# Performance work log

Measured on AMD Instinct MI355X. Metric: run time of the kernel, lower is better.

The kernel has to match this reference:

```python
import jax, jax.numpy as jnp
import numpy as np

B, N, D_IN, D_OUT, H, W = 2, 2048, 1024, 1024, 16, 64
DH = D_OUT // H


def setup_inputs() -> dict:
    key = jax.random.key(0)
    ks = jax.random.split(key, 6)
    x = jax.random.normal(ks[0], (B, N, D_IN), dtype=jnp.float32)
    s_in = 1.0 / np.sqrt(D_IN)
    s_out = 1.0 / np.sqrt(D_OUT)
    wq = jax.random.normal(ks[1], (D_IN, D_OUT), dtype=jnp.float32) * s_in
    wk = jax.random.normal(ks[2], (D_IN, D_OUT), dtype=jnp.float32) * s_in
    wv = jax.random.normal(ks[3], (D_IN, D_OUT), dtype=jnp.float32) * s_in
    wo = jax.random.normal(ks[4], (D_OUT, D_OUT), dtype=jnp.float32) * s_out
    # sparse global tokens: every 256th token is global
    global_attention = (jnp.arange(N)[None, :] % 256 == 0) & jnp.ones((B, 1), bool)
    return {"x": x, "wq": wq, "wk": wk, "wv": wv, "wo": wo,
            "global_attention": global_attention}


def _mask(global_attention):
    # True = masked out. Causal local window + global rows/cols unmasked.
    i = jnp.arange(N)[:, None]
    j = jnp.arange(N)[None, :]
    allowed = (i - j < W) & (i >= j)          # causal sliding window
    local_mask = ~allowed                      # [N, N], True = masked
    g = global_attention                       # [B, N] bool
    # global token j clears row j and column j of the mask
    global_clear = g[:, :, None] | g[:, None, :]   # [B, N, N]
    return local_mask[None, :, :] & ~global_clear  # [B, N, N]


def reference(x, wq, wk, wv, wo, global_attention):
    b, n, _ = x.shape
    q = (x @ wq).reshape(b, n, H, DH).transpose(0, 2, 1, 3)  # [b,h,n,dh]
    k = (x @ wk).reshape(b, n, H, DH).transpose(0, 2, 1, 3)
    v = (x @ wv).reshape(b, n, H, DH).transpose(0, 2, 1, 3)
    scores = jnp.einsum('bhqd,bhkd->bhqk', q, k) / jnp.sqrt(jnp.float32(DH))
    mask = _mask(global_attention)[:, None, :, :]            # [b,1,n,n]
    scores = jnp.where(mask, -jnp.inf, scores)
    attn = jax.nn.softmax(scores, axis=-1)
    ctx = jnp.einsum('bhqk,bhkd->bqhd', attn, v).reshape(b, n, D_OUT)
    return ctx @ wo
```

## Files before the change

kernel.cpp:

```cpp
#include <hip/hip_runtime.h>


using u16 = unsigned short;
using u32 = unsigned int;

typedef __attribute__((ext_vector_type(8))) short bf16x8;
typedef __attribute__((ext_vector_type(4))) float f32x4;

__device__ __forceinline__ float b2f(u16 s) {
  union { u32 u; float f; } x; x.u = ((u32)s) << 16; return x.f;
}
__device__ __forceinline__ u16 f2b(float f) {
  union { float f; u32 u; } x; x.f = f;
  u32 r = (x.u + 0x7fffu + ((x.u >> 16) & 1u)) >> 16;
  return (u16)r;
}

__global__ __launch_bounds__(256) void k_pre(const float* __restrict__ x,
                                             u16* __restrict__ xb,
                                             const float* __restrict__ wq,
                                             const float* __restrict__ wk,
                                             const float* __restrict__ wv,
                                             const float* __restrict__ wo,
                                             u16* __restrict__ wqkvT,
                                             u16* __restrict__ woT) {
  __shared__ float tile[64][65];
  const int bid = blockIdx.x;
  if (bid < 2048) {
    int idx = (bid * 256 + threadIdx.x) * 8;
    float4 a = *(const float4*)(x + idx);
    float4 b = *(const float4*)(x + idx + 4);
    uint4 o;
    o.x = (u32)f2b(a.x) | ((u32)f2b(a.y) << 16);
    o.y = (u32)f2b(a.z) | ((u32)f2b(a.w) << 16);
    o.z = (u32)f2b(b.x) | ((u32)f2b(b.y) << 16);
    o.w = (u32)f2b(b.z) | ((u32)f2b(b.w) << 16);
    *(uint4*)(xb + idx) = o;
  } else {
    const int id = bid - 2048;
    const int z = id >> 8, xy = id & 255;
    const float* src = (z == 0) ? wq : (z == 1) ? wk : (z == 2) ? wv : wo;
    u16* dst = (z < 3) ? (wqkvT + ((size_t)z << 20)) : woT;
    const int n0 = (xy & 15) * 64, k0 = (xy >> 4) * 64;
    const int tx = threadIdx.x & 63, ty = threadIdx.x >> 6;
    #pragma unroll
    for (int r = 0; r < 64; r += 4)
      tile[r + ty][tx] = src[(size_t)(k0 + r + ty) * 1024 + n0 + tx];
    __syncthreads();
    #pragma unroll
    for (int r = 0; r < 64; r += 4)
      dst[(size_t)(n0 + r + ty) * 1024 + k0 + tx] = f2b(tile[tx][r + ty]);
  }
}

__device__ __forceinline__ void gload16(const u16* g, u16* l) {
  __builtin_amdgcn_global_load_lds((const __attribute__((address_space(1))) void*)g,
                                   (__attribute__((address_space(3))) void*)l, 16, 0, 0);
}

__global__ __launch_bounds__(512, 2) void k_qkv256(const u16* __restrict__ A,
                                                   const u16* __restrict__ Bt,
                                                   u16* __restrict__ C) {
  __shared__ __attribute__((aligned(16))) u16 lds[57344];
  const int K = 1024, N = 3072, NT = 16;
  const int t = threadIdx.x;
  const int wid = t >> 6, lane = t & 63;
  const int l4 = lane >> 4, l16 = lane & 15;
  const int qr = wid >> 1, qc = wid & 1;
  const int d = blockIdx.y * gridDim.x + blockIdx.x;
  const int qq = (gridDim.x * gridDim.y) >> 3;
  const int tau = (d & 7) * qq + (d >> 3);
  const int bn = tau % gridDim.x, bm = tau / gridDim.x;
  const u16* Ab = A + (size_t)bm * 256 * K;
  const u16* Bb = Bt + (size_t)bn * 192 * K;
  const int rowbase = wid * 8 + (lane >> 3);
  const int qcg = rowbase >> 5, rrb = rowbase & 31;
  const int scc = ((lane & 7) ^ ((lane >> 3) & 7)) << 3;
  const int rsw = (l16 & 7);
  f32x4 acc[3][4][2] = {};
  bf16x8 af[4][2], bf[2][2];

  #define STG_A(BUF, KT, H)                                                        \
    { u16* lb = lds + (BUF) * 16384 + (H) * 8192 + (wid << 9);                     \
      _Pragma("unroll")                                                            \
      for (int i = 0; i < 2; ++i)                                                  \
        gload16(Ab + (size_t)((H) * 128 + i * 64 + rowbase) * K + (KT) * 64 + scc, \
                lb + i * 4096); }

  #define STG_B1(BUF, KT, I)                                                       \
    { u16* lb = lds + 32768 + (BUF) * 12288 + (I) * 4096 + (wid << 9);             \
      gload16(Bb + (size_t)(qcg * 96 + (I) * 32 + rrb) * K + (KT) * 64 + scc, lb); }

  #define LOAD_A(AS)                                                               \
    { _Pragma("unroll")                                                            \
      for (int m = 0; m < 4; ++m) {                                                \
        const int ro = qr * 64 + m * 16 + l16;                                     \
        _Pragma("unroll")                                                          \
        for (int ks = 0; ks < 2; ++ks)                                             \
          af[m][ks] = *(const bf16x8*)&(AS)[ro * 64 + (((ks * 4 + l4) ^ rsw) << 3)]; \
      } }

  #define LOAD_B(BS, NH)                                                           \
    { _Pragma("unroll")                                                            \
      for (int n = 0; n < 2; ++n) {                                                \
        const int po = (NH) * 64 + qc * 32 + n * 16 + l16;                         \
        _Pragma("unroll")                                                          \
        for (int ks = 0; ks < 2; ++ks)                                             \
          bf[n][ks] = *(const bf16x8*)&(BS)[po * 64 + (((ks * 4 + l4) ^ rsw) << 3)]; \
      } }

  #define QUAD(NH)                                                                 \
    { __builtin_amdgcn_s_setprio(1);                                               \
      _Pragma("unroll")                                                            \
      for (int m = 0; m < 4; ++m)                                                  \
        _Pragma("unroll")                                                          \
        for (int n = 0; n < 2; ++n) {                                              \
          f32x4 c = acc[NH][m][n];                                                 \
          c = __builtin_amdgcn_mfma_f32_16x16x32_bf16(af[m][0], bf[n][0], c, 0, 0, 0); \
          c = __builtin_amdgcn_mfma_f32_16x16x32_bf16(af[m][1], bf[n][1], c, 0, 0, 0); \
          acc[NH][m][n] = c;                                                       \
        }                                                                          \
      __builtin_amdgcn_s_setprio(0); }

  STG_A(0, 0, 0); STG_A(0, 0, 1);
  STG_B1(0, 0, 0); STG_B1(0, 0, 1); STG_B1(0, 0, 2);
  STG_A(1, 1, 0); STG_A(1, 1, 1);
  STG_B1(1, 1, 0);
  asm volatile("s_waitcnt vmcnt(5)" ::: "memory");
  __builtin_amdgcn_s_barrier();

  for (int tt = 0; tt < NT; ++tt) {
    const int beta = tt & 1;
    const u16* As = lds + beta * 16384;
    const u16* Bs = lds + 32768 + beta * 12288;
    LOAD_A(As);
    LOAD_B(Bs, 0);
    if (tt + 1 < NT) STG_B1(beta ^ 1, tt + 1, 1);
    __builtin_amdgcn_s_barrier();
    QUAD(0);
    __builtin_amdgcn_s_barrier();
    LOAD_B(Bs, 1);
    if (tt + 1 < NT) STG_B1(beta ^ 1, tt + 1, 2);
    __builtin_amdgcn_s_barrier();
    QUAD(1);
    __builtin_amdgcn_s_barrier();
    LOAD_B(Bs, 2);
    if (tt + 2 < NT) {
      STG_A(beta, tt + 2, 0);
      STG_A(beta, tt + 2, 1);
      STG_B1(beta, tt + 2, 0);
    }
    __builtin_amdgcn_s_barrier();
    QUAD(2);
    if (tt + 2 < NT)      asm volatile("s_waitcnt vmcnt(5)" ::: "memory");
    else if (tt + 1 < NT) asm volatile("s_waitcnt vmcnt(0)" ::: "memory");
    __builtin_amdgcn_s_barrier();
  }
  #undef STG_A
  #undef STG_B1
  #undef LOAD_A
  #undef LOAD_B
  #undef QUAD

  #pragma unroll
  for (int nh = 0; nh < 3; ++nh)
    #pragma unroll
    for (int m = 0; m < 4; ++m) {
      const int row0 = bm * 256 + qr * 64 + m * 16 + l4 * 4;
      #pragma unroll
      for (int n = 0; n < 2; ++n) {
        const int col = bn * 192 + qc * 96 + nh * 32 + n * 16 + l16;
        #pragma unroll
        for (int r = 0; r < 4; ++r)
          C[(size_t)(row0 + r) * N + col] = f2b(acc[nh][m][n][r]);
      }
    }
}

__global__ __launch_bounds__(512, 2) void k_out(const u16* __restrict__ A,
                                                const u16* __restrict__ Bt,
                                                float* __restrict__ C,
                                                const float* __restrict__ gpart,
                                                u16* __restrict__ ctxw) {
  __shared__ __attribute__((aligned(16))) u16 lds[32768];
  const int K = 1024, N = 1024, NT = 16;
  const int t = threadIdx.x;
  const int wid = t >> 6, lane = t & 63;
  const int l4 = lane >> 4, l16 = lane & 15;
  const int qr = wid >> 2, qc = wid & 3;
  const int d = blockIdx.y * gridDim.x + blockIdx.x;
  const int qq = (gridDim.x * gridDim.y) >> 3;
  const int tau = (d & 7) * qq + (d >> 3);
  const int bn = tau % gridDim.x, bm = tau / gridDim.x;
  const u16* Ab = A + (size_t)bm * 128 * K;
  const u16* Bb = Bt + (size_t)bn * 128 * K;
  const int rowbase = wid * 8 + (lane >> 3);
  const int qcg = rowbase >> 4, rrb = rowbase & 15;
  const int scc = ((lane & 7) ^ ((lane >> 3) & 7)) << 3;
  const int rsw = (l16 & 7);
  f32x4 acc[2][4] = {};
  bf16x8 af[4][2], bf[2][2];

  if ((bm & 1) == 0) {
    if (t < 256) {
      const int bb = bm >> 4;
      const int irow = (bm & 15) * 128;
      const int row8 = (bm & 15) >> 1;
      const int h = t >> 4;
      const int d0 = (t & 15) * 4;
      const float* g0 = gpart + ((size_t)(bb * 16 + h) * 32) * 520;
      float o0 = 0.f, o1 = 0.f, o2 = 0.f, o3 = 0.f, ls = 0.f;
      for (int q = 0; q < 32; ++q) {
        const float4 v = *(const float4*)(g0 + q * 520 + row8 * 64 + d0);
        o0 += v.x; o1 += v.y; o2 += v.z; o3 += v.w;
        ls += g0[q * 520 + 512 + row8];
      }
      const float inv = 1.f / ls;
      u16* cw = ctxw + ((size_t)(bb * 2048 + irow)) * 1024 + h * 64 + d0;
      cw[0] = f2b(o0 * inv); cw[1] = f2b(o1 * inv);
      cw[2] = f2b(o2 * inv); cw[3] = f2b(o3 * inv);
    }
    __syncthreads();
  }

  #define OSTG_A(BUF, KT)                                                          \
    { u16* lb = lds + (BUF) * 8192 + (wid << 9);                                   \
      _Pragma("unroll")                                                            \
      for (int i = 0; i < 2; ++i)                                                  \
        gload16(Ab + (size_t)(i * 64 + rowbase) * K + (KT) * 64 + scc,             \
                lb + i * 4096); }

  #define OSTG_B(BUF, KT)                                                          \
    { u16* lb = lds + 16384 + (BUF) * 8192 + (wid << 9);                           \
      _Pragma("unroll")                                                            \
      for (int nf = 0; nf < 2; ++nf)                                               \
        gload16(Bb + (size_t)(qcg * 32 + nf * 16 + rrb) * K + (KT) * 64 + scc,     \
                lb + nf * 4096); }

  #define OLOAD()                                                                  \
    { _Pragma("unroll")                                                            \
      for (int m = 0; m < 4; ++m) {                                                \
        const int ro = qr * 64 + m * 16 + l16;                                     \
        _Pragma("unroll")                                                          \
        for (int ks = 0; ks < 2; ++ks)                                             \
          af[m][ks] = *(const bf16x8*)&As[ro * 64 + (((ks * 4 + l4) ^ rsw) << 3)]; \
      }                                                                            \
      _Pragma("unroll")                                                            \
      for (int nf = 0; nf < 2; ++nf) {                                             \
        const int po = nf * 64 + qc * 16 + l16;                                    \
        _Pragma("unroll")                                                          \
        for (int ks = 0; ks < 2; ++ks)                                             \
          bf[nf][ks] = *(const bf16x8*)&Bs[po * 64 + (((ks * 4 + l4) ^ rsw) << 3)]; \
      } }

  OSTG_A(0, 0); OSTG_B(0, 0);
  OSTG_A(1, 1); OSTG_B(1, 1);
  asm volatile("s_waitcnt vmcnt(4)" ::: "memory");
  __builtin_amdgcn_s_barrier();

  for (int tt = 0; tt < NT; ++tt) {
    const int beta = tt & 1;
    const u16* As = lds + beta * 8192;
    const u16* Bs = lds + 16384 + beta * 8192;
    OLOAD();
    asm volatile("s_waitcnt lgkmcnt(0)" ::: "memory");
    __builtin_amdgcn_s_barrier();
    if (tt + 2 < NT) { OSTG_A(beta, tt + 2); OSTG_B(beta, tt + 2); }
    __builtin_amdgcn_s_setprio(1);
    #pragma unroll
    for (int nf = 0; nf < 2; ++nf)
      #pragma unroll
      for (int m = 0; m < 4; ++m) {
        f32x4 c = acc[nf][m];
        c = __builtin_amdgcn_mfma_f32_16x16x32_bf16(af[m][0], bf[nf][0], c, 0, 0, 0);
        c = __builtin_amdgcn_mfma_f32_16x16x32_bf16(af[m][1], bf[nf][1], c, 0, 0, 0);
        acc[nf][m] = c;
      }
    __builtin_amdgcn_s_setprio(0);
    if (tt + 2 < NT)      asm volatile("s_waitcnt vmcnt(4)" ::: "memory");
    else if (tt + 1 < NT) asm volatile("s_waitcnt vmcnt(0)" ::: "memory");
    __builtin_amdgcn_s_barrier();
  }
  #undef OSTG_A
  #undef OSTG_B
  #undef OLOAD

  #pragma unroll
  for (int nf = 0; nf < 2; ++nf)
    #pragma unroll
    for (int m = 0; m < 4; ++m) {
      const int row0 = bm * 128 + qr * 64 + m * 16 + l4 * 4;
      const int col = bn * 128 + qc * 32 + nf * 16 + l16;
      #pragma unroll
      for (int r = 0; r < 4; ++r)
        C[(size_t)(row0 + r) * N + col] = acc[nf][m][r];
    }
}

__global__ __launch_bounds__(256) void k_attn_tile(const u16* __restrict__ qkv,
                                                   u16* __restrict__ ctx,
                                                   float* __restrict__ gpart) {
  __shared__ u16 buf[26880];
  __shared__ u16 Qgs[16 * 72];
  __shared__ u16 Pgs[16 * 72];
  __shared__ float lred[4][16];
  u16* Qs = buf;
  u16* Ks = buf + 4608;
  u16* Vt = buf + 16128;
  u16* Ps = buf;

  const int t = threadIdx.x, wid = t >> 6, lane = t & 63;
  const int l4 = lane >> 4, l16 = lane & 15;
  const int qt = blockIdx.x, h = blockIdx.y, b = blockIdx.z;
  const int q0 = qt * 64;
  const int kbase = q0 - 64;
  const size_t base = (size_t)b * 2048 * 3072;
  const u16* Qg = qkv + base + h * 64;
  const u16* Kg = qkv + base + 1024 + h * 64;
  const u16* Vg = qkv + base + 2048 + h * 64;

  for (int s = t; s < 512; s += 256) {
    int r = s >> 3, c = (s & 7) * 8;
    *(uint4*)&Qs[r * 72 + c] = *(const uint4*)&Qg[(size_t)(q0 + r) * 3072 + c];
  }
  if (t < 128) {
    int r = t >> 3, c = (t & 7) * 8;
    if (r < 8) {
      *(uint4*)&Qgs[r * 72 + c] = *(const uint4*)&Qg[(size_t)(r * 256) * 3072 + c];
    } else {
      uint4 z = {0, 0, 0, 0};
      *(uint4*)&Qgs[r * 72 + c] = z;
    }
  }
  for (int s = t; s < 1088; s += 256) {
    int r = s >> 3, c = (s & 7) * 8;
    int j = (r < 128) ? max(kbase + r, 0) : (r - 128) * 256;
    *(uint4*)&Ks[r * 72 + c] = *(const uint4*)&Kg[(size_t)j * 3072 + c];
  }
  for (int s = t; s < 1088; s += 256) {
    int r = s >> 3, c = (s & 7) * 8;
    int j = (r < 128) ? max(kbase + r, 0) : (r - 128) * 256;
    uint4 v = *(const uint4*)&Vg[(size_t)j * 3072 + c];
    const u16* pv = (const u16*)&v;
    const int ch = r >> 3;
    #pragma unroll
    for (int e8 = 0; e8 < 8; ++e8) {
      const int d = c + e8;
      const int kd = ((d >> 3) ^ d) & 7;
      const int chs = (ch < 16) ? (ch ^ kd) : ch;
      Vt[d * 168 + chs * 8 + (r & 7)] = pv[e8];
    }
  }
  for (int z = t; z < 64 * 24; z += 256) {
    int d = z / 24, j = 136 + z % 24;
    Vt[d * 168 + j] = 0;
  }
  __syncthreads();

  f32x4 sa[10] = {};
  #pragma unroll
  for (int ks = 0; ks < 2; ++ks) {
    bf16x8 qa = *(const bf16x8*)&Qs[(wid * 16 + l16) * 72 + ks * 32 + l4 * 8];
    #pragma unroll
    for (int n = 0; n < 10; ++n) {
      bf16x8 kb = *(const bf16x8*)&Ks[(n * 16 + l16) * 72 + ks * 32 + l4 * 8];
      sa[n] = __builtin_amdgcn_mfma_f32_16x16x32_bf16(qa, kb, sa[n], 0, 0, 0);
    }
  }

  f32x4 sg = {};
  #pragma unroll
  for (int ks = 0; ks < 2; ++ks) {
    bf16x8 qa = *(const bf16x8*)&Qgs[l16 * 72 + ks * 32 + l4 * 8];
    bf16x8 kb = *(const bf16x8*)&Ks[(64 + wid * 16 + l16) * 72 + ks * 32 + l4 * 8];
    sg = __builtin_amdgcn_mfma_f32_16x16x32_bf16(qa, kb, sg, 0, 0, 0);
  }
  #pragma unroll
  for (int r = 0; r < 4; ++r) {
    float p = __expf(sg[r] * 0.125f);
    sg[r] = p;
    #pragma unroll
    for (int o = 1; o < 16; o <<= 1) p += __shfl_xor(p, o);
    if (l16 == 0) lred[wid][l4 * 4 + r] = p;
  }
  #pragma unroll
  for (int r = 0; r < 4; ++r)
    Pgs[(l4 * 4 + r) * 72 + wid * 16 + l16] = f2b(sg[r]);

  const int qi0 = wid * 16 + l4 * 4;
  #pragma unroll
  for (int n = 0; n < 10; ++n) {
    const int jc = n * 16 + l16;
    #pragma unroll
    for (int r = 0; r < 4; ++r) {
      const int qi = qi0 + r;
      bool allowed;
      if (n < 8) {
        const int kr = kbase + jc;
        allowed = (jc > qi) && (jc <= qi + 64) && (kr >= 0) && ((kr & 255) != 0);
      } else {
        allowed = (jc < 136);
      }
      sa[n][r] = allowed ? sa[n][r] * 0.125f : -1e30f;
    }
  }

  float m[4], l[4];
  #pragma unroll
  for (int r = 0; r < 4; ++r) {
    float mx = sa[0][r];
    #pragma unroll
    for (int n = 1; n < 10; ++n) mx = fmaxf(mx, sa[n][r]);
    #pragma unroll
    for (int o = 1; o < 16; o <<= 1) mx = fmaxf(mx, __shfl_xor(mx, o));
    m[r] = mx;
    l[r] = 0.f;
  }
  #pragma unroll
  for (int n = 0; n < 10; ++n)
    #pragma unroll
    for (int r = 0; r < 4; ++r) {
      float p = __expf(sa[n][r] - m[r]);
      sa[n][r] = p;
      l[r] += p;
    }
  #pragma unroll
  for (int r = 0; r < 4; ++r)
    #pragma unroll
    for (int o = 1; o < 16; o <<= 1) l[r] += __shfl_xor(l[r], o);

  __syncthreads();

  u16* Pw = Ps + wid * (16 * 168);
  #pragma unroll
  for (int n = 0; n < 10; ++n)
    #pragma unroll
    for (int r = 0; r < 4; ++r)
      Pw[(l4 * 4 + r) * 168 + n * 16 + l16] = f2b(sa[n][r]);
  __syncthreads();

  f32x4 o[4] = {};
  #pragma unroll
  for (int ks = 0; ks < 5; ++ks) {
    bf16x8 pa = *(const bf16x8*)&Pw[l16 * 168 + ks * 32 + l4 * 8];
    #pragma unroll
    for (int dt = 0; dt < 4; ++dt) {
      const int dvo = dt * 16 + l16;
      const int kdo = ((dvo >> 3) ^ dvo) & 7;
      const int ch = ks * 4 + l4;
      const int chs = (ch < 16) ? (ch ^ kdo) : ch;
      bf16x8 vb = *(const bf16x8*)&Vt[dvo * 168 + chs * 8];
      o[dt] = __builtin_amdgcn_mfma_f32_16x16x32_bf16(pa, vb, o[dt], 0, 0, 0);
    }
  }

  f32x4 og = {};
  {
    const int dV = wid * 16 + l16;
    const int kdg = ((dV >> 3) ^ dV) & 7;
    #pragma unroll
    for (int ks = 0; ks < 2; ++ks) {
      bf16x8 pa = *(const bf16x8*)&Pgs[l16 * 72 + ks * 32 + l4 * 8];
      const int chs = (8 + ks * 4 + l4) ^ kdg;
      bf16x8 vb = *(const bf16x8*)&Vt[dV * 168 + chs * 8];
      og = __builtin_amdgcn_mfma_f32_16x16x32_bf16(pa, vb, og, 0, 0, 0);
    }
  }
  float* gp = gpart + ((size_t)(b * 16 + h) * 32 + qt) * 520;
  #pragma unroll
  for (int r = 0; r < 4; ++r) {
    int row = l4 * 4 + r;
    if (row < 8) gp[row * 64 + wid * 16 + l16] = og[r];
  }
  if (t < 8) gp[512 + t] = lred[0][t] + lred[1][t] + lred[2][t] + lred[3][t];

  #pragma unroll
  for (int r = 0; r < 4; ++r) {
    const int q = q0 + qi0 + r;
    if ((q & 255) == 0) continue;
    const float inv = 1.0f / l[r];
    #pragma unroll
    for (int dt = 0; dt < 4; ++dt)
      ctx[(size_t)(b * 2048 + q) * 1024 + h * 64 + dt * 16 + l16] = f2b(o[dt][r] * inv);
  }
}

extern "C" void kernel_launch(void* const* d_in, const int* in_sizes, int n_in,
                              void* d_out, int out_size, void* d_ws, size_t ws_size,
                              hipStream_t stream) {
  (void)in_sizes; (void)n_in; (void)out_size; (void)ws_size;
  const float* x  = (const float*)d_in[0];
  const float* wq = (const float*)d_in[1];
  const float* wk = (const float*)d_in[2];
  const float* wv = (const float*)d_in[3];
  const float* wo = (const float*)d_in[4];
  char* ws = (char*)d_ws;
  u16* xb    = (u16*)(ws);
  u16* qkv   = (u16*)(ws + (8u  << 20));
  u16* ctx   = (u16*)(ws + (32u << 20));
  u16* wqkvT = (u16*)(ws + (40u << 20));
  u16* woT   = (u16*)(ws + (46u << 20));
  float* gpart = (float*)(ws);

  k_pre<<<3072, 256, 0, stream>>>(x, xb, wq, wk, wv, wo, wqkvT, woT);
  k_qkv256<<<dim3(16, 16), 512, 0, stream>>>(xb, wqkvT, qkv);
  k_attn_tile<<<dim3(32, 16, 2), 256, 0, stream>>>(qkv, ctx, gpart);
  k_out<<<dim3(8, 32), 512, 0, stream>>>(ctx, woT, (float*)d_out, gpart, ctx);
}
```

Measured before the change: 79.94 us.

## Fuse fp32-to-bf16 conversion of x into the QKV GEMM A-tile staging

The separate pass that converted x to bf16 in a workspace is removed, so k_pre now only transposes and converts the weights. The QKV GEMM instead loads fp32 x tiles into registers one k-step ahead, converts them with the packed v_cvt_pk_bf16_f32 instruction, and stores them to LDS in the same swizzled layout that the async global-to-LDS copies used before. This avoids writing and re-reading a bf16 copy of x and shrinks the pre-pass grid. In exchange the GEMM reads twice the bytes for A across all column blocks, holds extra registers for the prefetch (with a risk of spills under the 512x2 launch bound), and depends on hand-tuned vmcnt/lgkmcnt waits.

```diff
diff --git a/kernel.cpp b/kernel.cpp
--- a/kernel.cpp
+++ b/kernel.cpp
@@ -15,42 +15,30 @@
   u32 r = (x.u + 0x7fffu + ((x.u >> 16) & 1u)) >> 16;
   return (u16)r;
 }
-
-__global__ __launch_bounds__(256) void k_pre(const float* __restrict__ x,
-                                             u16* __restrict__ xb,
-                                             const float* __restrict__ wq,
+__device__ __forceinline__ u32 cvtpk(float lo, float hi) {
+  u32 r; asm("v_cvt_pk_bf16_f32 %0, %1, %2" : "=v"(r) : "v"(lo), "v"(hi)); return r;
+}
+
+__global__ __launch_bounds__(256) void k_pre(const float* __restrict__ wq,
                                              const float* __restrict__ wk,
                                              const float* __restrict__ wv,
                                              const float* __restrict__ wo,
                                              u16* __restrict__ wqkvT,
                                              u16* __restrict__ woT) {
   __shared__ float tile[64][65];
-  const int bid = blockIdx.x;
-  if (bid < 2048) {
-    int idx = (bid * 256 + threadIdx.x) * 8;
-    float4 a = *(const float4*)(x + idx);
-    float4 b = *(const float4*)(x + idx + 4);
-    uint4 o;
-    o.x = (u32)f2b(a.x) | ((u32)f2b(a.y) << 16);
-    o.y = (u32)f2b(a.z) | ((u32)f2b(a.w) << 16);
-    o.z = (u32)f2b(b.x) | ((u32)f2b(b.y) << 16);
-    o.w = (u32)f2b(b.z) | ((u32)f2b(b.w) << 16);
-    *(uint4*)(xb + idx) = o;
-  } else {
-    const int id = bid - 2048;
-    const int z = id >> 8, xy = id & 255;
-    const float* src = (z == 0) ? wq : (z == 1) ? wk : (z == 2) ? wv : wo;
-    u16* dst = (z < 3) ? (wqkvT + ((size_t)z << 20)) : woT;
-    const int n0 = (xy & 15) * 64, k0 = (xy >> 4) * 64;
-    const int tx = threadIdx.x & 63, ty = threadIdx.x >> 6;
-    #pragma unroll
-    for (int r = 0; r < 64; r += 4)
-      tile[r + ty][tx] = src[(size_t)(k0 + r + ty) * 1024 + n0 + tx];
-    __syncthreads();
-    #pragma unroll
-    for (int r = 0; r < 64; r += 4)
-      dst[(size_t)(n0 + r + ty) * 1024 + k0 + tx] = f2b(tile[tx][r + ty]);
-  }
+  const int id = blockIdx.x;
+  const int z = id >> 8, xy = id & 255;
+  const float* src = (z == 0) ? wq : (z == 1) ? wk : (z == 2) ? wv : wo;
+  u16* dst = (z < 3) ? (wqkvT + ((size_t)z << 20)) : woT;
+  const int n0 = (xy & 15) * 64, k0 = (xy >> 4) * 64;
+  const int tx = threadIdx.x & 63, ty = threadIdx.x >> 6;
+  #pragma unroll
+  for (int r = 0; r < 64; r += 4)
+    tile[r + ty][tx] = src[(size_t)(k0 + r + ty) * 1024 + n0 + tx];
+  __syncthreads();
+  #pragma unroll
+  for (int r = 0; r < 64; r += 4)
+    dst[(size_t)(n0 + r + ty) * 1024 + k0 + tx] = f2b(tile[tx][r + ty]);
 }
 
 __device__ __forceinline__ void gload16(const u16* g, u16* l) {
@@ -58,7 +46,7 @@
                                    (__attribute__((address_space(3))) void*)l, 16, 0, 0);
 }
 
-__global__ __launch_bounds__(512, 2) void k_qkv256(const u16* __restrict__ A,
+__global__ __launch_bounds__(512, 2) void k_qkv256(const float* __restrict__ X,
                                                    const u16* __restrict__ Bt,
                                                    u16* __restrict__ C) {
   __shared__ __attribute__((aligned(16))) u16 lds[57344];
@@ -71,7 +59,7 @@
   const int qq = (gridDim.x * gridDim.y) >> 3;
   const int tau = (d & 7) * qq + (d >> 3);
   const int bn = tau % gridDim.x, bm = tau / gridDim.x;
-  const u16* Ab = A + (size_t)bm * 256 * K;
+  const float* Ax = X + (size_t)bm * 256 * K;
   const u16* Bb = Bt + (size_t)bn * 192 * K;
   const int rowbase = wid * 8 + (lane >> 3);
   const int qcg = rowbase >> 5, rrb = rowbase & 31;
@@ -79,13 +67,32 @@
   const int rsw = (l16 & 7);
   f32x4 acc[3][4][2] = {};
   bf16x8 af[4][2], bf[2][2];
-
-  #define STG_A(BUF, KT, H)                                                        \
-    { u16* lb = lds + (BUF) * 16384 + (H) * 8192 + (wid << 9);                     \
-      _Pragma("unroll")                                                            \
-      for (int i = 0; i < 2; ++i)                                                  \
-        gload16(Ab + (size_t)((H) * 128 + i * 64 + rowbase) * K + (KT) * 64 + scc, \
-                lb + i * 4096); }
+  float4 fa[2][2][2];
+
+  #define ISSUE_AF(KT)                                                             \
+    { _Pragma("unroll")                                                            \
+      for (int H = 0; H < 2; ++H)                                                  \
+        _Pragma("unroll")                                                          \
+        for (int i = 0; i < 2; ++i) {                                              \
+          const float* ap = Ax + (size_t)(H * 128 + i * 64 + rowbase) * K          \
+                               + (KT) * 64 + scc;                                  \
+          fa[H][i][0] = *(const float4*)ap;                                        \
+          fa[H][i][1] = *(const float4*)(ap + 4);                                  \
+        } }
+
+  #define WRITE_AF(BUF)                                                            \
+    { _Pragma("unroll")                                                            \
+      for (int H = 0; H < 2; ++H)                                                  \
+        _Pragma("unroll")                                                          \
+        for (int i = 0; i < 2; ++i) {                                              \
+          union { u32 w[4]; uint4 v; } u_;                                         \
+          u_.w[0] = cvtpk(fa[H][i][0].x, fa[H][i][0].y);                           \
+          u_.w[1] = cvtpk(fa[H][i][0].z, fa[H][i][0].w);                           \
+          u_.w[2] = cvtpk(fa[H][i][1].x, fa[H][i][1].y);                           \
+          u_.w[3] = cvtpk(fa[H][i][1].z, fa[H][i][1].w);                           \
+          *(uint4*)&lds[(BUF) * 16384 + H * 8192 + i * 4096 + (wid << 9)           \
+                        + lane * 8] = u_.v;                                        \
+        } }
 
   #define STG_B1(BUF, KT, I)                                                       \
     { u16* lb = lds + 32768 + (BUF) * 12288 + (I) * 4096 + (wid << 9);             \
@@ -122,11 +129,21 @@
         }                                                                          \
       __builtin_amdgcn_s_setprio(0); }
 
-  STG_A(0, 0, 0); STG_A(0, 0, 1);
+  ISSUE_AF(0);
+  __builtin_amdgcn_sched_barrier(0);
+  WRITE_AF(0);
+  __builtin_amdgcn_sched_barrier(0);
+  ISSUE_AF(1);
+  __builtin_amdgcn_sched_barrier(0);
+  WRITE_AF(1);
+  __builtin_amdgcn_sched_barrier(0);
   STG_B1(0, 0, 0); STG_B1(0, 0, 1); STG_B1(0, 0, 2);
-  STG_A(1, 1, 0); STG_A(1, 1, 1);
   STG_B1(1, 1, 0);
-  asm volatile("s_waitcnt vmcnt(5)" ::: "memory");
+  __builtin_amdgcn_sched_barrier(0);
+  ISSUE_AF(2);
+  __builtin_amdgcn_sched_barrier(0);
+  asm volatile("s_waitcnt vmcnt(9)" ::: "memory");
+  asm volatile("s_waitcnt lgkmcnt(0)" ::: "memory");
   __builtin_amdgcn_s_barrier();
 
   for (int tt = 0; tt < NT; ++tt) {
@@ -145,18 +162,21 @@
     QUAD(1);
     __builtin_amdgcn_s_barrier();
     LOAD_B(Bs, 2);
-    if (tt + 2 < NT) {
-      STG_A(beta, tt + 2, 0);
-      STG_A(beta, tt + 2, 1);
-      STG_B1(beta, tt + 2, 0);
-    }
+    if (tt + 2 < NT) WRITE_AF(beta);
+    __builtin_amdgcn_sched_barrier(0);
+    if (tt + 3 < NT) ISSUE_AF(tt + 3);
+    __builtin_amdgcn_sched_barrier(0);
+    if (tt + 2 < NT) STG_B1(beta, tt + 2, 0);
     __builtin_amdgcn_s_barrier();
     QUAD(2);
-    if (tt + 2 < NT)      asm volatile("s_waitcnt vmcnt(5)" ::: "memory");
+    if (tt + 3 < NT)      asm volatile("s_waitcnt vmcnt(9)" ::: "memory");
+    else if (tt + 2 < NT) asm volatile("s_waitcnt vmcnt(1)" ::: "memory");
     else if (tt + 1 < NT) asm volatile("s_waitcnt vmcnt(0)" ::: "memory");
-    __builtin_amdgcn_s_barrier();
-  }
-  #undef STG_A
+    asm volatile("s_waitcnt lgkmcnt(0)" ::: "memory");
+    __builtin_amdgcn_s_barrier();
+  }
+  #undef ISSUE_AF
+  #undef WRITE_AF
   #undef STG_B1
   #undef LOAD_A
   #undef LOAD_B
@@ -495,15 +515,14 @@
   const float* wv = (const float*)d_in[3];
   const float* wo = (const float*)d_in[4];
   char* ws = (char*)d_ws;
-  u16* xb    = (u16*)(ws);
   u16* qkv   = (u16*)(ws + (8u  << 20));
   u16* ctx   = (u16*)(ws + (32u << 20));
   u16* wqkvT = (u16*)(ws + (40u << 20));
   u16* woT   = (u16*)(ws + (46u << 20));
   float* gpart = (float*)(ws);
 
-  k_pre<<<3072, 256, 0, stream>>>(x, xb, wq, wk, wv, wo, wqkvT, woT);
-  k_qkv256<<<dim3(16, 16), 512, 0, stream>>>(xb, wqkvT, qkv);
+  k_pre<<<1024, 256, 0, stream>>>(wq, wk, wv, wo, wqkvT, woT);
+  k_qkv256<<<dim3(16, 16), 512, 0, stream>>>(x, wqkvT, qkv);
   k_attn_tile<<<dim3(32, 16, 2), 256, 0, stream>>>(qkv, ctx, gpart);
   k_out<<<dim3(8, 32), 512, 0, stream>>>(ctx, woT, (float*)d_out, gpart, ctx);
 }
```

Result: slower. 83.98 us (+5.0%).
